# Optimization experiments

Hardware: AMD Instinct MI355X
Metric: run time of the kernel (lower is better)

Reference implementation:

```python
import jax, jax.numpy as jnp
import numpy as np

N_NODES = 100000
N_EDGES = 1600000
IN_FEATS = 256
OUT_FEATS = 128
GAMMA = 1.0


def setup_inputs() -> dict:
    key = jax.random.key(0)
    k1, k2, k3, k4, k5 = jax.random.split(key, 5)
    glorot = np.sqrt(6.0 / (IN_FEATS + OUT_FEATS)).astype(np.float32)
    feat = jax.random.normal(k1, (N_NODES, IN_FEATS), dtype=jnp.float32)
    W_mean = jax.random.uniform(k2, (IN_FEATS, OUT_FEATS), dtype=jnp.float32, minval=-glorot, maxval=glorot)
    W_var = jax.random.uniform(k3, (IN_FEATS, OUT_FEATS), dtype=jnp.float32, minval=-glorot, maxval=glorot)
    src = jax.random.randint(k4, (N_EDGES,), 0, N_NODES, dtype=jnp.int64 if jax.config.jax_enable_x64 else jnp.int32)
    dst = jax.random.randint(k5, (N_EDGES,), 0, N_NODES, dtype=jnp.int64 if jax.config.jax_enable_x64 else jnp.int32)
    return {"feat": feat, "W_mean": W_mean, "W_var": W_var, "src": src, "dst": dst}


def reference(feat, W_mean, W_var, src, dst):
    # dense projections + relu (no bias, as bias=False)
    mean = jax.nn.relu(jnp.matmul(feat, W_mean))   # [N, F]
    var = jax.nn.relu(jnp.matmul(feat, W_var))     # [N, F]
    attention = jnp.exp(-GAMMA * var)
    # in-degrees from dst edge endpoints, clamped to >= 1
    degs = jax.ops.segment_sum(jnp.ones_like(dst, dtype=jnp.float32), dst, num_segments=N_NODES)
    degs = jnp.clip(degs, 1.0)
    norm1 = (degs ** -0.5)[:, None]                # [N, 1] = D^{-1/2}
    norm2 = norm1 * norm1                          # [N, 1] = D^{-1}
    m_msg = mean * attention * norm1
    v_msg = var * attention * attention * norm2
    # copy_src + sum aggregation (SpMM over edge list)
    mean_agg = jax.ops.segment_sum(m_msg[src], dst, num_segments=N_NODES) * norm1
    var_agg = jax.ops.segment_sum(v_msg[src], dst, num_segments=N_NODES) * norm2
    return mean_agg, var_agg
```

## Files before the change

kernel.cpp:

```cpp
#include <hip/hip_runtime.h>
#include <hip/hip_bf16.h>

#define N_NODES 100000
#define N_EDGES 1600000
#define OUTF 128
#define INF 256
#define SCAN_CHUNK 1024
#define SCAN_BLOCKS 98
#define M_TILES 6250

typedef _Float16 f16;
typedef _Float16 half8 __attribute__((ext_vector_type(8)));
typedef _Float16 half2v __attribute__((ext_vector_type(2)));
typedef float floatx4 __attribute__((ext_vector_type(4)));

__global__ void count_rank_kernel(const int* __restrict__ dst, int E,
                                  int* __restrict__ deg, int* __restrict__ rank) {
    int i = blockIdx.x * blockDim.x + threadIdx.x;
    if (i < E) rank[i] = atomicAdd(&deg[dst[i]], 1);
}

__global__ __launch_bounds__(256) void scan_partial_kernel(const int* __restrict__ deg, int n,
                                                           int* __restrict__ partial) {
    __shared__ int red[256];
    int b = blockIdx.x, t = threadIdx.x;
    int base = b * SCAN_CHUNK;
    int s = 0;
    for (int i = t; i < SCAN_CHUNK; i += 256) {
        int idx = base + i;
        if (idx < n) s += deg[idx];
    }
    red[t] = s;
    __syncthreads();
    for (int off = 128; off > 0; off >>= 1) {
        if (t < off) red[t] += red[t + off];
        __syncthreads();
    }
    if (t == 0) partial[b] = red[0];
}

__global__ __launch_bounds__(128) void scan_top_kernel(int* __restrict__ partial, int nb,
                                                       int* __restrict__ row_start, int n) {
    __shared__ int sc[128];
    int t = threadIdx.x;
    int v = (t < nb) ? partial[t] : 0;
    sc[t] = v;
    __syncthreads();
    for (int off = 1; off < 128; off <<= 1) {
        int val = sc[t];
        int add = (t >= off) ? sc[t - off] : 0;
        __syncthreads();
        sc[t] = val + add;
        __syncthreads();
    }
    if (t < nb) partial[t] = sc[t] - v;
    if (t == 127) row_start[n] = sc[127];
}

__global__ __launch_bounds__(256) void scan_final_kernel(const int* __restrict__ deg, int n,
                                                         const int* __restrict__ partial,
                                                         int* __restrict__ row_start,
                                                         float* __restrict__ norm1,
                                                         float* __restrict__ norm2) {
    __shared__ int sc[256];
    int b = blockIdx.x, t = threadIdx.x;
    int base = b * SCAN_CHUNK + t * 4;
    int v[4];
    int tsum = 0;
#pragma unroll
    for (int j = 0; j < 4; j++) {
        int idx = base + j;
        v[j] = (idx < n) ? deg[idx] : 0;
        tsum += v[j];
    }
    sc[t] = tsum;
    __syncthreads();
    for (int off = 1; off < 256; off <<= 1) {
        int val = sc[t];
        int add = (t >= off) ? sc[t - off] : 0;
        __syncthreads();
        sc[t] = val + add;
        __syncthreads();
    }
    int run = sc[t] - tsum + partial[b];
#pragma unroll
    for (int j = 0; j < 4; j++) {
        int idx = base + j;
        if (idx < n) {
            row_start[idx] = run;
            float d = (float)(v[j] > 0 ? v[j] : 1);
            norm1[idx] = rsqrtf(d);
            norm2[idx] = 1.0f / d;
            run += v[j];
        }
    }
}

__global__ void scatter_edges_kernel(const int* __restrict__ src, const int* __restrict__ dst,
                                     const int* __restrict__ rank,
                                     const int* __restrict__ row_start,
                                     int E, int* __restrict__ srcs_sorted) {
    int i = blockIdx.x * blockDim.x + threadIdx.x;
    if (i < E) {
        srcs_sorted[row_start[dst[i]] + rank[i]] = src[i];
    }
}

__global__ __launch_bounds__(256) void convert_B_kernel(const float* __restrict__ Wm,
                                                        const float* __restrict__ Wv,
                                                        f16* __restrict__ Bt) {
    int k = threadIdx.x;
    int ng = blockIdx.x;
    int g = ng >> 4, i = ng & 15;
    int w = g >> 2, cg = g & 3;
    int col = w * 32 + (cg & 1) * 16 + i;
    const float* srcW = (cg >= 2) ? Wv : Wm;
    Bt[ng * 256 + k] = (f16)srcW[k * 128 + col];
}

__global__ __launch_bounds__(256, 2) void proj_mfma_kernel(const float* __restrict__ feat,
                                                           const f16* __restrict__ Bt,
                                                           const float* __restrict__ norm1,
                                                           const float* __restrict__ norm2,
                                                           f16* __restrict__ msg) {
    int tid = threadIdx.x;
    int w = tid >> 6;
    int lane = tid & 63;
    int quad = lane >> 4;
    int l15 = lane & 15;

    half8 b[4][8];
#pragma unroll
    for (int cg = 0; cg < 4; cg++) {
        int g = w * 4 + cg;
        const f16* bp = Bt + (size_t)(g * 16 + l15) * 256 + quad * 8;
#pragma unroll
        for (int kf = 0; kf < 8; kf++) {
            b[cg][kf] = *(const half8*)(bp + kf * 32);
        }
    }

    for (int t = blockIdx.x; t < M_TILES; t += gridDim.x) {
        int m0 = t * 16;
        half8 a[8];
        const float* ap = feat + (size_t)(m0 + l15) * 256 + quad * 8;
#pragma unroll
        for (int kf = 0; kf < 8; kf++) {
            floatx4 f0 = *(const floatx4*)(ap + kf * 32);
            floatx4 f1 = *(const floatx4*)(ap + kf * 32 + 4);
            half8 h;
            h[0] = (f16)f0.x; h[1] = (f16)f0.y; h[2] = (f16)f0.z; h[3] = (f16)f0.w;
            h[4] = (f16)f1.x; h[5] = (f16)f1.y; h[6] = (f16)f1.z; h[7] = (f16)f1.w;
            a[kf] = h;
        }

        floatx4 acc[4];
#pragma unroll
        for (int cg = 0; cg < 4; cg++) acc[cg] = (floatx4){0.f, 0.f, 0.f, 0.f};

#pragma unroll
        for (int cg = 0; cg < 4; cg++) {
#pragma unroll
            for (int kf = 0; kf < 8; kf++) {
                acc[cg] = __builtin_amdgcn_mfma_f32_16x16x32_f16(a[kf], b[cg][kf], acc[cg], 0, 0, 0);
            }
        }

#pragma unroll
        for (int cg = 0; cg < 2; cg++) {
            int col = w * 32 + cg * 16 + l15;
#pragma unroll
            for (int r = 0; r < 4; r++) {
                int row = quad * 4 + r;
                int node = m0 + row;
                float m = fmaxf(acc[cg][r], 0.f);
                float v = fmaxf(acc[cg + 2][r], 0.f);
                float att = __expf(-v);
                float s1 = norm1[node];
                float s2 = norm2[node];
                msg[(size_t)node * 256 + col] = (f16)(m * att * s1);
                msg[(size_t)node * 256 + 128 + col] = (f16)(v * att * att * s2);
            }
        }
    }
}

__global__ __launch_bounds__(256) void agg_kernel(const int* __restrict__ row_start,
                                                  const int* __restrict__ srcs,
                                                  const f16* __restrict__ msg,
                                                  const float* __restrict__ norm1,
                                                  const float* __restrict__ norm2,
                                                  float* __restrict__ out_mean,
                                                  float* __restrict__ out_var) {
    int d = blockIdx.x * 4 + (threadIdx.x >> 6);
    int lane = threadIdx.x & 63;
    int s0 = row_start[d];
    int s1 = row_start[d + 1];
    float am0 = 0.f, am1 = 0.f, av0 = 0.f, av1 = 0.f;
    int i = s0;
    for (; i + 3 < s1; i += 4) {
        int sa = srcs[i], sb = srcs[i + 1], sc = srcs[i + 2], sd = srcs[i + 3];
        half2v ma = *(const half2v*)(msg + (size_t)sa * 256 + lane * 2);
        half2v va = *(const half2v*)(msg + (size_t)sa * 256 + 128 + lane * 2);
        half2v mb = *(const half2v*)(msg + (size_t)sb * 256 + lane * 2);
        half2v vb = *(const half2v*)(msg + (size_t)sb * 256 + 128 + lane * 2);
        half2v mc = *(const half2v*)(msg + (size_t)sc * 256 + lane * 2);
        half2v vc = *(const half2v*)(msg + (size_t)sc * 256 + 128 + lane * 2);
        half2v md = *(const half2v*)(msg + (size_t)sd * 256 + lane * 2);
        half2v vd = *(const half2v*)(msg + (size_t)sd * 256 + 128 + lane * 2);
        am0 += (float)ma[0] + (float)mb[0] + (float)mc[0] + (float)md[0];
        am1 += (float)ma[1] + (float)mb[1] + (float)mc[1] + (float)md[1];
        av0 += (float)va[0] + (float)vb[0] + (float)vc[0] + (float)vd[0];
        av1 += (float)va[1] + (float)vb[1] + (float)vc[1] + (float)vd[1];
    }
    for (; i < s1; i++) {
        int sa = srcs[i];
        half2v ma = *(const half2v*)(msg + (size_t)sa * 256 + lane * 2);
        half2v va = *(const half2v*)(msg + (size_t)sa * 256 + 128 + lane * 2);
        am0 += (float)ma[0];
        am1 += (float)ma[1];
        av0 += (float)va[0];
        av1 += (float)va[1];
    }
    float k1 = norm1[d], k2 = norm2[d];
    float2 om = make_float2(am0 * k1, am1 * k1);
    float2 ov = make_float2(av0 * k2, av1 * k2);
    *(float2*)(out_mean + (size_t)d * 128 + lane * 2) = om;
    *(float2*)(out_var + (size_t)d * 128 + lane * 2) = ov;
}

extern "C" void kernel_launch(void* const* d_in, const int* in_sizes, int n_in,
                              void* d_out, int out_size, void* d_ws, size_t ws_size,
                              hipStream_t stream) {
    const float* feat = (const float*)d_in[0];
    const float* Wm = (const float*)d_in[1];
    const float* Wv = (const float*)d_in[2];
    const int* src = (const int*)d_in[3];
    const int* dst = (const int*)d_in[4];
    float* out = (float*)d_out;

    const int N = N_NODES;
    const int E = N_EDGES;

    char* wsp = (char*)d_ws;
    auto carve = [&](size_t bytes) {
        char* p = wsp;
        wsp += (bytes + 255) & ~(size_t)255;
        return p;
    };
    f16* msg = (f16*)carve((size_t)N * 256 * sizeof(f16));
    f16* Bt = (f16*)carve((size_t)256 * 256 * sizeof(f16));
    int* srcs_sorted = (int*)carve((size_t)E * 4);
    int* rank = (int*)carve((size_t)E * 4);
    int* deg = (int*)carve((size_t)N * 4);
    int* row_start = (int*)carve((size_t)(N + 1) * 4);
    float* norm1 = (float*)carve((size_t)N * 4);
    float* norm2 = (float*)carve((size_t)N * 4);
    int* partial = (int*)carve(128 * 4);

    hipMemsetAsync(deg, 0, (size_t)N * 4, stream);

    count_rank_kernel<<<(E + 255) / 256, 256, 0, stream>>>(dst, E, deg, rank);
    convert_B_kernel<<<256, 256, 0, stream>>>(Wm, Wv, Bt);
    scan_partial_kernel<<<SCAN_BLOCKS, 256, 0, stream>>>(deg, N, partial);
    scan_top_kernel<<<1, 128, 0, stream>>>(partial, SCAN_BLOCKS, row_start, N);
    scan_final_kernel<<<SCAN_BLOCKS, 256, 0, stream>>>(deg, N, partial, row_start, norm1, norm2);
    scatter_edges_kernel<<<(E + 255) / 256, 256, 0, stream>>>(src, dst, rank, row_start, E,
                                                              srcs_sorted);
    proj_mfma_kernel<<<1250, 256, 0, stream>>>(feat, Bt, norm1, norm2, msg);
    agg_kernel<<<N / 4, 256, 0, stream>>>(row_start, srcs_sorted, msg, norm1, norm2,
                                          out, out + (size_t)N * OUTF);
}
```

Measured before the change: 491.3 us.

## Interleave mean/var messages and split projection columns across block pairs

The message buffer now stores each node's mean and var values interleaved per column. The aggregation kernel can then fetch one half4 per lane per edge instead of two half2 loads, and it unrolls the edge loop by 8 instead of 4. The projection kernel splits output columns between pairs of blocks, so each wave holds half as many B fragments. It launches twice as many blocks with a higher occupancy bound and hoists the norm loads ahead of the MFMA loop. The trade-off is that every block pair re-reads and re-converts the same feature rows, doubling reads of the large feat input.

```diff
diff --git a/kernel.cpp b/kernel.cpp
--- a/kernel.cpp
+++ b/kernel.cpp
@@ -11,6 +11,7 @@
 
 typedef _Float16 f16;
 typedef _Float16 half8 __attribute__((ext_vector_type(8)));
+typedef _Float16 half4 __attribute__((ext_vector_type(4)));
 typedef _Float16 half2v __attribute__((ext_vector_type(2)));
 typedef float floatx4 __attribute__((ext_vector_type(4)));
 
@@ -112,13 +113,13 @@
     int k = threadIdx.x;
     int ng = blockIdx.x;
     int g = ng >> 4, i = ng & 15;
-    int w = g >> 2, cg = g & 3;
-    int col = w * 32 + (cg & 1) * 16 + i;
-    const float* srcW = (cg >= 2) ? Wv : Wm;
+    int ch = g >> 3, w = (g >> 1) & 3, cg = g & 1;
+    int col = ch * 64 + w * 16 + i;
+    const float* srcW = cg ? Wv : Wm;
     Bt[ng * 256 + k] = (f16)srcW[k * 128 + col];
 }
 
-__global__ __launch_bounds__(256, 2) void proj_mfma_kernel(const float* __restrict__ feat,
+__global__ __launch_bounds__(256, 3) void proj_mfma_kernel(const float* __restrict__ feat,
                                                            const f16* __restrict__ Bt,
                                                            const float* __restrict__ norm1,
                                                            const float* __restrict__ norm2,
@@ -128,11 +129,13 @@
     int lane = tid & 63;
     int quad = lane >> 4;
     int l15 = lane & 15;
-
-    half8 b[4][8];
-#pragma unroll
-    for (int cg = 0; cg < 4; cg++) {
-        int g = w * 4 + cg;
+    int ch = blockIdx.x & 1;
+    int tbase = blockIdx.x >> 1;
+
+    half8 b[2][8];
+#pragma unroll
+    for (int cg = 0; cg < 2; cg++) {
+        int g = ch * 8 + w * 2 + cg;
         const f16* bp = Bt + (size_t)(g * 16 + l15) * 256 + quad * 8;
 #pragma unroll
         for (int kf = 0; kf < 8; kf++) {
@@ -140,7 +143,9 @@
         }
     }
 
-    for (int t = blockIdx.x; t < M_TILES; t += gridDim.x) {
+    int col = ch * 64 + w * 16 + l15;
+
+    for (int t = tbase; t < M_TILES; t += 1250) {
         int m0 = t * 16;
         half8 a[8];
         const float* ap = feat + (size_t)(m0 + l15) * 256 + quad * 8;
@@ -154,33 +159,32 @@
             a[kf] = h;
         }
 
-        floatx4 acc[4];
-#pragma unroll
-        for (int cg = 0; cg < 4; cg++) acc[cg] = (floatx4){0.f, 0.f, 0.f, 0.f};
-
-#pragma unroll
-        for (int cg = 0; cg < 4; cg++) {
-#pragma unroll
-            for (int kf = 0; kf < 8; kf++) {
-                acc[cg] = __builtin_amdgcn_mfma_f32_16x16x32_f16(a[kf], b[cg][kf], acc[cg], 0, 0, 0);
-            }
-        }
-
-#pragma unroll
-        for (int cg = 0; cg < 2; cg++) {
-            int col = w * 32 + cg * 16 + l15;
-#pragma unroll
-            for (int r = 0; r < 4; r++) {
-                int row = quad * 4 + r;
-                int node = m0 + row;
-                float m = fmaxf(acc[cg][r], 0.f);
-                float v = fmaxf(acc[cg + 2][r], 0.f);
-                float att = __expf(-v);
-                float s1 = norm1[node];
-                float s2 = norm2[node];
-                msg[(size_t)node * 256 + col] = (f16)(m * att * s1);
-                msg[(size_t)node * 256 + 128 + col] = (f16)(v * att * att * s2);
-            }
+        float s1r[4], s2r[4];
+#pragma unroll
+        for (int r = 0; r < 4; r++) {
+            int node = m0 + quad * 4 + r;
+            s1r[r] = norm1[node];
+            s2r[r] = norm2[node];
+        }
+
+        floatx4 acc0 = (floatx4){0.f, 0.f, 0.f, 0.f};
+        floatx4 acc1 = (floatx4){0.f, 0.f, 0.f, 0.f};
+#pragma unroll
+        for (int kf = 0; kf < 8; kf++) {
+            acc0 = __builtin_amdgcn_mfma_f32_16x16x32_f16(a[kf], b[0][kf], acc0, 0, 0, 0);
+            acc1 = __builtin_amdgcn_mfma_f32_16x16x32_f16(a[kf], b[1][kf], acc1, 0, 0, 0);
+        }
+
+#pragma unroll
+        for (int r = 0; r < 4; r++) {
+            int node = m0 + quad * 4 + r;
+            float m = fmaxf(acc0[r], 0.f);
+            float v = fmaxf(acc1[r], 0.f);
+            float att = __expf(-v);
+            half2v pr;
+            pr[0] = (f16)(m * att * s1r[r]);
+            pr[1] = (f16)(v * att * att * s2r[r]);
+            *(half2v*)(msg + (size_t)node * 256 + col * 2) = pr;
         }
     }
 }
@@ -198,29 +202,26 @@
     int s1 = row_start[d + 1];
     float am0 = 0.f, am1 = 0.f, av0 = 0.f, av1 = 0.f;
     int i = s0;
-    for (; i + 3 < s1; i += 4) {
-        int sa = srcs[i], sb = srcs[i + 1], sc = srcs[i + 2], sd = srcs[i + 3];
-        half2v ma = *(const half2v*)(msg + (size_t)sa * 256 + lane * 2);
-        half2v va = *(const half2v*)(msg + (size_t)sa * 256 + 128 + lane * 2);
-        half2v mb = *(const half2v*)(msg + (size_t)sb * 256 + lane * 2);
-        half2v vb = *(const half2v*)(msg + (size_t)sb * 256 + 128 + lane * 2);
-        half2v mc = *(const half2v*)(msg + (size_t)sc * 256 + lane * 2);
-        half2v vc = *(const half2v*)(msg + (size_t)sc * 256 + 128 + lane * 2);
-        half2v md = *(const half2v*)(msg + (size_t)sd * 256 + lane * 2);
-        half2v vd = *(const half2v*)(msg + (size_t)sd * 256 + 128 + lane * 2);
-        am0 += (float)ma[0] + (float)mb[0] + (float)mc[0] + (float)md[0];
-        am1 += (float)ma[1] + (float)mb[1] + (float)mc[1] + (float)md[1];
-        av0 += (float)va[0] + (float)vb[0] + (float)vc[0] + (float)vd[0];
-        av1 += (float)va[1] + (float)vb[1] + (float)vc[1] + (float)vd[1];
+    for (; i + 7 < s1; i += 8) {
+        half4 h[8];
+#pragma unroll
+        for (int j = 0; j < 8; j++) {
+            h[j] = *(const half4*)(msg + (size_t)srcs[i + j] * 256 + lane * 4);
+        }
+#pragma unroll
+        for (int j = 0; j < 8; j++) {
+            am0 += (float)h[j][0];
+            av0 += (float)h[j][1];
+            am1 += (float)h[j][2];
+            av1 += (float)h[j][3];
+        }
     }
     for (; i < s1; i++) {
-        int sa = srcs[i];
-        half2v ma = *(const half2v*)(msg + (size_t)sa * 256 + lane * 2);
-        half2v va = *(const half2v*)(msg + (size_t)sa * 256 + 128 + lane * 2);
-        am0 += (float)ma[0];
-        am1 += (float)ma[1];
-        av0 += (float)va[0];
-        av1 += (float)va[1];
+        half4 ha = *(const half4*)(msg + (size_t)srcs[i] * 256 + lane * 4);
+        am0 += (float)ha[0];
+        av0 += (float)ha[1];
+        am1 += (float)ha[2];
+        av1 += (float)ha[3];
     }
     float k1 = norm1[d], k2 = norm2[d];
     float2 om = make_float2(am0 * k1, am1 * k1);
@@ -267,7 +268,7 @@
     scan_final_kernel<<<SCAN_BLOCKS, 256, 0, stream>>>(deg, N, partial, row_start, norm1, norm2);
     scatter_edges_kernel<<<(E + 255) / 256, 256, 0, stream>>>(src, dst, rank, row_start, E,
                                                               srcs_sorted);
-    proj_mfma_kernel<<<1250, 256, 0, stream>>>(feat, Bt, norm1, norm2, msg);
+    proj_mfma_kernel<<<2500, 256, 0, stream>>>(feat, Bt, norm1, norm2, msg);
     agg_kernel<<<N / 4, 256, 0, stream>>>(row_start, srcs_sorted, msg, norm1, norm2,
                                           out, out + (size_t)N * OUTF);
 }
```

After: 491.8 us. Within noise of the previous version (+0.1%).
